# Kernel tuning notes

Measured on AMD Instinct MI355X. Metric: run time of the kernel, lower is better.

Reference implementation:

```python
import jax, jax.numpy as jnp
import numpy as np
from jax import lax

N, C, H, W = 1, 3, 480, 640
K_LCN = 9
K_ASW = 12
SIGMA_OMEGA = 2.0
LCN_WEIGHT = 0.5
OCC_WEIGHT = 0.1
LN2 = 0.6931


def _box_filter(x, k):
    # depthwise kxk mean filter, zero ('same') padding — matches F.conv2d(groups=3)
    w = jnp.ones((C, 1, k, k), x.dtype) / (k * k)
    return lax.conv_general_dilated(
        x, w, (1, 1), [(k // 2, k // 2)] * 2,
        dimension_numbers=('NCHW', 'OIHW', 'NCHW'), feature_group_count=C)


def _lcn(img, k=K_LCN):
    mean = _box_filter(img, k)
    msq = _box_filter(img ** 2, k)
    std = jnp.sqrt(jax.nn.relu(msq - mean ** 2)) * (k * k) / (k * k - 1)
    return (img - mean) / (std + 1e-5), std


def _sample_x(img, x):
    # grid_sample with identity y and x-only shift reduces to horizontal linear
    # interpolation with zero padding (align_corners=False pixel-center math).
    Wd = img.shape[-1]
    x0 = jnp.floor(x)
    w1 = x - x0
    x0i = x0.astype(jnp.int32)
    def gather(xi):
        valid = ((xi >= 0) & (xi < Wd)).astype(img.dtype)
        return jnp.take_along_axis(img, jnp.clip(xi, 0, Wd - 1), axis=-1) * valid
    return gather(x0i) * (1 - w1) + gather(x0i + 1) * w1


def _resample(img, disp_other, disp_guide, sign):
    # sample img and disp_other at x = j + sign*disp_guide (left view: sign=-1)
    xs = jnp.arange(W, dtype=img.dtype) + sign * disp_guide  # [N,1,H,W]
    recon_img = _sample_x(img, jnp.broadcast_to(xs, img.shape))
    recon_disp = _sample_x(disp_other, xs)
    return recon_img, recon_disp


def _asw(guide, cost, k=K_ASW, sigma=SIGMA_OMEGA):
    # adaptive support-weight (bilateral) aggregation over a kxk window,
    # zero-padded, window offsets -k//2 .. k//2-1 (even k, as in the original)
    pad = k // 2
    gp = jnp.pad(guide, ((0, 0), (0, 0), (pad, pad), (pad, pad)))
    cp = jnp.pad(cost, ((0, 0), (0, 0), (pad, pad), (pad, pad)))
    shape = guide.shape
    def body(carry, idx):
        wg, ca = carry
        i = idx // k
        j = idx % k
        gs = lax.dynamic_slice(gp, (0, 0, i, j), shape)
        cs = lax.dynamic_slice(cp, (0, 0, i, j), shape)
        t = jnp.exp(-jnp.abs(guide - gs) / sigma)
        return (wg + t, ca + t * cs), None
    init = (jnp.zeros(shape, guide.dtype), jnp.zeros(shape, guide.dtype))
    (wg, ca), _ = lax.scan(body, init, jnp.arange(k * k, dtype=jnp.int32))
    return ca / wg


def _ce_ones_target(p):
    # CrossEntropyLoss(mean) with logits [1-p, p] and target class 1 everywhere
    logits = jnp.concatenate([1.0 - p, p], axis=1)  # [N,2,H,W]
    ls = jax.nn.log_softmax(logits, axis=1)
    return -jnp.mean(ls[:, 1])


def _forward(left_img, right_img, dispmap_left, dispmap_right, weight):
    recon_img_right, recon_disp_right = _resample(right_img, dispmap_right, dispmap_left, -1.0)
    recon_img_left, recon_disp_left = _resample(left_img, dispmap_left, dispmap_right, 1.0)

    losses_left_photo = jnp.abs(left_img - recon_img_right)
    losses_right_photo = jnp.abs(right_img - recon_img_left)

    rir_lcn, _ = _lcn(recon_img_right)
    ril_lcn, _ = _lcn(recon_img_left)
    l_lcn, l_std = _lcn(left_img)
    r_lcn, r_std = _lcn(right_img)
    losses_left_lcn = _asw(left_img, jnp.abs((l_lcn - rir_lcn) * l_std))
    # NOTE: original uses left_img as the ASW guide for the right loss too
    losses_right_lcn = _asw(left_img, jnp.abs((r_lcn - ril_lcn) * r_std))

    losses_left = (1 - LCN_WEIGHT) * losses_left_photo + LCN_WEIGHT * losses_left_lcn
    losses_right = (1 - LCN_WEIGHT) * losses_right_photo + LCN_WEIGHT * losses_right_lcn

    p_left = jnp.exp(-LN2 * jnp.abs(dispmap_left - recon_disp_right))   # [N,1,H,W]
    p_right = jnp.exp(-LN2 * jnp.abs(dispmap_right - recon_disp_left))

    loss_invalid = _ce_ones_target(p_left) + _ce_ones_target(p_right)

    mask_left = (p_left > 0.5).astype(losses_left.dtype)    # broadcasts over C=3
    mask_right = (p_right > 0.5).astype(losses_right.dtype)
    loss_valid = (jnp.sum(losses_left * mask_left) / (C * jnp.sum(mask_left) + 1e-6)
                  + jnp.sum(losses_right * mask_right) / (C * jnp.sum(mask_right) + 1e-6))

    return weight * ((1 - OCC_WEIGHT) * loss_valid + OCC_WEIGHT * loss_invalid)


def setup_inputs() -> dict:
    key = jax.random.key(0)
    k1, k2, k3, k4, k5 = jax.random.split(key, 5)
    return {
        'left_img': jax.random.uniform(k1, (N, C, H, W), dtype=jnp.float32),
        'right_img': jax.random.uniform(k2, (N, C, H, W), dtype=jnp.float32),
        'dispmap_left': jax.random.uniform(k3, (N, 1, H, W), dtype=jnp.float32) * 32.0,
        'dispmap_right': jax.random.uniform(k4, (N, 1, H, W), dtype=jnp.float32) * 32.0,
        'dispmap_gt': jax.random.uniform(k5, (N, 1, H, W), dtype=jnp.float32) * 32.0,
        'brk': 0,
        'weight': jnp.asarray(1.0, dtype=jnp.float32),
    }


def reference(left_img, right_img, dispmap_left, dispmap_right, dispmap_gt, brk, weight):
    # dispmap_gt and brk are accepted but unused by the original forward math
    return _forward(left_img, right_img, dispmap_left, dispmap_right, weight)
```

## Files before the change

### kernel.cpp

```cpp
#include <hip/hip_runtime.h>
#include <math.h>

#define HH 480
#define WW 640
#define HW (HH*WW)

#define NB1 1200
#define NB3 3600

__device__ __forceinline__ unsigned bf16rne(float f) {
    unsigned u = __float_as_uint(f);
    return (u + 0x7fffu + ((u >> 16) & 1u)) >> 16;
}


__device__ __forceinline__ float sample1(const float* __restrict__ row, float x) {
    float x0 = floorf(x);
    float w1 = x - x0;
    int xi = (int)x0;
    float v0 = (xi >= 0 && xi < WW) ? row[xi] : 0.f;
    float v1 = (xi + 1 >= 0 && xi + 1 < WW) ? row[xi + 1] : 0.f;
    return v0 * (1.f - w1) + v1 * w1;
}

__global__ __launch_bounds__(256) void k_resample(
    const float* __restrict__ left, const float* __restrict__ right,
    const float* __restrict__ dispL, const float* __restrict__ dispR,
    float* __restrict__ rir, float* __restrict__ ril,
    unsigned char* __restrict__ maskb, float* __restrict__ part1)
{
    __shared__ float red[4][6];
    int tid = threadIdx.x;
    int idx = blockIdx.x * blockDim.x + tid;
    int h = idx / WW;
    int w = idx - h * WW;
    float dL = dispL[idx];
    float dR = dispR[idx];
    float xl = (float)w - dL;
    float xr = (float)w + dR;
    float photoL = 0.f, photoR = 0.f;
    #pragma unroll
    for (int c = 0; c < 3; ++c) {
        float rv = sample1(right + c*HW + h*WW, xl);
        float lv = sample1(left  + c*HW + h*WW, xr);
        rir[c*HW + idx] = rv;
        ril[c*HW + idx] = lv;
        photoL += fabsf(left [c*HW + idx] - rv);
        photoR += fabsf(right[c*HW + idx] - lv);
    }
    float rdr = sample1(dispR + h*WW, xl);
    float rdl = sample1(dispL + h*WW, xr);
    float pl = __expf(-0.6931f * fabsf(dL - rdr));
    float pr = __expf(-0.6931f * fabsf(dR - rdl));
    float mL = (pl > 0.5f) ? 1.f : 0.f;
    float mR = (pr > 0.5f) ? 1.f : 0.f;
    maskb[idx] = (unsigned char)((mL > 0.f ? 1u : 0u) | (mR > 0.f ? 2u : 0u));

    float vals[6];
    vals[0] = 0.5f * photoL * mL;
    vals[1] = mL;
    vals[2] = 0.5f * photoR * mR;
    vals[3] = mR;
    vals[4] = log1pf(__expf(1.f - 2.f * pl));
    vals[5] = log1pf(__expf(1.f - 2.f * pr));

    int lane = tid & 63, wave = tid >> 6;
    #pragma unroll
    for (int k = 0; k < 6; ++k) {
        float v = vals[k];
        #pragma unroll
        for (int off = 32; off > 0; off >>= 1) v += __shfl_down(v, off);
        if (lane == 0) red[wave][k] = v;
    }
    __syncthreads();
    if (tid < 6)
        part1[blockIdx.x * 8 + tid] =
            red[0][tid] + red[1][tid] + red[2][tid] + red[3][tid];
}


__global__ __launch_bounds__(256) void k_lcnpack(
    const float* __restrict__ left, const float* __restrict__ right,
    const float* __restrict__ rir, const float* __restrict__ ril,
    unsigned* __restrict__ epem,
    unsigned short* __restrict__ cl16, unsigned short* __restrict__ cr16)
{
    __shared__ float raw[2][16][40];
    __shared__ float2 hsp[2][16][32];
    int tx = threadIdx.x, ty = threadIdx.y;
    int tid = ty * 32 + tx;
    int gx0 = blockIdx.x * 32, gy0 = blockIdx.y * 8;
    int side = blockIdx.z & 1, ch = blockIdx.z >> 1;
    const float* __restrict__ A = (side ? right : left) + ch*HW;
    const float* __restrict__ B = (side ? ril   : rir) + ch*HW;

    for (int e = tid; e < 2*16*40; e += 256) {
        int a   = e / 640;
        int rem = e - a * 640;
        int r   = rem / 40;
        int x   = rem - r * 40;
        int gy = gy0 + r - 4, gx = gx0 + x - 4;
        float v = 0.f;
        if ((unsigned)gy < (unsigned)HH && (unsigned)gx < (unsigned)WW)
            v = (a ? B : A)[gy*WW + gx];
        ((float*)raw)[e] = v;
    }
    __syncthreads();

    {
        int f   = tid;
        int a   = f >> 7;
        int rem = f & 127;
        int r   = rem >> 3;
        int x0  = (rem & 7) * 4;
        const float* row = &raw[a][r][x0];
        float4 p0 = *(const float4*)(row);
        float4 p1 = *(const float4*)(row + 4);
        float4 p2 = *(const float4*)(row + 8);
        float v[12] = {p0.x, p0.y, p0.z, p0.w, p1.x, p1.y, p1.z, p1.w,
                       p2.x, p2.y, p2.z, p2.w};
        float sq[12];
        #pragma unroll
        for (int i = 0; i < 12; ++i) sq[i] = v[i] * v[i];
        float s0 = v[0]+v[1]+v[2]+v[3]+v[4]+v[5]+v[6]+v[7]+v[8];
        float q0 = sq[0]+sq[1]+sq[2]+sq[3]+sq[4]+sq[5]+sq[6]+sq[7]+sq[8];
        float s1 = s0 - v[0] + v[9];
        float q1 = q0 - sq[0] + sq[9];
        float s2 = s1 - v[1] + v[10];
        float q2 = q1 - sq[1] + sq[10];
        float s3 = s2 - v[2] + v[11];
        float q3 = q2 - sq[2] + sq[11];
        float4* out = (float4*)&hsp[a][r][x0];
        out[0] = make_float4(s0, q0, s1, q1);
        out[1] = make_float4(s2, q2, s3, q3);
    }
    __syncthreads();

    int idx = ch*HW + (gy0 + ty) * WW + gx0 + tx;
    float SA = 0.f, SA2 = 0.f, SB = 0.f, SB2 = 0.f;
    #pragma unroll
    for (int dy = 0; dy < 9; ++dy) {
        float2 ha = hsp[0][ty + dy][tx];
        float2 hb = hsp[1][ty + dy][tx];
        SA  += ha.x;
        SA2 += ha.y;
        SB  += hb.x;
        SB2 += hb.y;
    }
    float meanA = SA * (1.f/81.f);
    float stdA  = sqrtf(fmaxf(SA2 * (1.f/81.f) - meanA * meanA, 0.f)) * (81.f/80.f);
    float lcnA  = (raw[0][ty + 4][tx + 4] - meanA) / (stdA + 1e-5f);
    float meanB = SB * (1.f/81.f);
    float stdB  = sqrtf(fmaxf(SB2 * (1.f/81.f) - meanB * meanB, 0.f)) * (81.f/80.f);
    float lcnB  = (raw[1][ty + 4][tx + 4] - meanB) / (stdB + 1e-5f);
    float cost  = fabsf((lcnA - lcnB) * stdA);
    if (side == 0) {
        float g = raw[0][ty + 4][tx + 4];
        epem[idx] = bf16rne(__expf(0.5f * g)) | (bf16rne(__expf(-0.5f * g)) << 16);
        cl16[idx] = (unsigned short)bf16rne(cost);
    } else {
        cr16[idx] = (unsigned short)bf16rne(cost);
    }
}


#define T3H 19
#define T3W 43

__global__ __launch_bounds__(64) void k_asw_reduce(
    const unsigned* __restrict__ epem,
    const unsigned short* __restrict__ cl16, const unsigned short* __restrict__ cr16,
    const unsigned char* __restrict__ maskb,
    float* __restrict__ part3)
{
    __shared__ float4 tile[T3H][T3W];
    int tx = threadIdx.x, ty = threadIdx.y;
    int tid = tx + 32 * ty;
    int c = blockIdx.z;
    int gx0 = blockIdx.x * 32, gy0 = blockIdx.y * 8;

    for (int e = tid; e < T3H * T3W; e += 64) {
        int r   = e / T3W;
        int x   = e - r * T3W;
        int gy = gy0 + r - 6, gx = gx0 + x - 6;
        float4 v = make_float4(1.f, 1.f, 0.f, 0.f);
        if ((unsigned)gy < (unsigned)HH && (unsigned)gx < (unsigned)WW) {
            int o = c*HW + gy*WW + gx;
            unsigned pe = epem[o];
            v.x = __uint_as_float(pe << 16);
            v.y = __uint_as_float(pe & 0xffff0000u);
            v.z = __uint_as_float((unsigned)cl16[o] << 16);
            v.w = __uint_as_float((unsigned)cr16[o] << 16);
        }
        tile[r][x] = v;
    }
    __syncthreads();

    int ty4 = 4 * ty;
    float epc[4], emc[4];
    #pragma unroll
    for (int i = 0; i < 4; ++i) {
        float4 cv = tile[ty4 + i + 6][tx + 6];
        epc[i] = cv.x;
        emc[i] = cv.y;
    }

    float wg[4] = {0.f,0.f,0.f,0.f}, aL[4] = {0.f,0.f,0.f,0.f}, aR[4] = {0.f,0.f,0.f,0.f};

    auto taprow = [&](int kap, int i0, int i1) {
        const float4* row = &tile[ty4 + kap][tx];
        #pragma unroll
        for (int dx = 0; dx < 12; ++dx) {
            float4 v = row[dx];
            #pragma unroll
            for (int i = 0; i < 4; ++i) {
                if (i >= i0 && i <= i1) {
                    float t = fminf(emc[i] * v.x, epc[i] * v.y);
                    wg[i] += t;
                    aL[i] = fmaf(t, v.z, aL[i]);
                    aR[i] = fmaf(t, v.w, aR[i]);
                }
            }
        }
    };

    taprow(0, 0, 0);
    taprow(1, 0, 1);
    taprow(2, 0, 2);
    for (int kap = 3; kap <= 11; ++kap)
        taprow(kap, 0, 3);
    taprow(12, 1, 3);
    taprow(13, 2, 3);
    taprow(14, 3, 3);

    float v0 = 0.f, v2 = 0.f;
    #pragma unroll
    for (int i = 0; i < 4; ++i) {
        int idx = (gy0 + ty4 + i) * WW + gx0 + tx;
        unsigned m = maskb[idx];
        float aswL = aL[i] / wg[i];
        float aswR = aR[i] / wg[i];
        if (m & 1u) v0 += 0.5f * aswL;
        if (m & 2u) v2 += 0.5f * aswR;
    }

    #pragma unroll
    for (int off = 32; off > 0; off >>= 1) {
        v0 += __shfl_down(v0, off);
        v2 += __shfl_down(v2, off);
    }
    if (tid == 0) {
        int bid = (blockIdx.z * gridDim.y + blockIdx.y) * gridDim.x + blockIdx.x;
        part3[bid * 8 + 0] = v0;
        part3[bid * 8 + 1] = v2;
    }
}


__global__ __launch_bounds__(256) void k_final(
    const float* __restrict__ part1, const float* __restrict__ part3,
    const float* __restrict__ weight, float* __restrict__ out)
{
    __shared__ float red[4][6];
    int tid = threadIdx.x;
    float v[6] = {0.f, 0.f, 0.f, 0.f, 0.f, 0.f};
    for (int b = tid; b < NB1; b += 256) {
        #pragma unroll
        for (int k = 0; k < 6; ++k) v[k] += part1[b * 8 + k];
    }
    for (int b = tid; b < NB3; b += 256) {
        v[0] += part3[b * 8 + 0];
        v[2] += part3[b * 8 + 1];
    }
    int lane = tid & 63, wave = tid >> 6;
    #pragma unroll
    for (int k = 0; k < 6; ++k) {
        float s = v[k];
        #pragma unroll
        for (int off = 32; off > 0; off >>= 1) s += __shfl_down(s, off);
        if (lane == 0) red[wave][k] = s;
    }
    __syncthreads();
    if (tid == 0) {
        float a[6];
        #pragma unroll
        for (int k = 0; k < 6; ++k)
            a[k] = red[0][k] + red[1][k] + red[2][k] + red[3][k];
        float loss_valid = a[0] / (3.f * a[1] + 1e-6f) + a[2] / (3.f * a[3] + 1e-6f);
        float loss_invalid = (a[4] + a[5]) * (1.f / (float)HW);
        out[0] = weight[0] * (0.9f * loss_valid + 0.1f * loss_invalid);
    }
}


extern "C" void kernel_launch(void* const* d_in, const int* in_sizes, int n_in,
                              void* d_out, int out_size, void* d_ws, size_t ws_size,
                              hipStream_t stream)
{
    const float* left  = (const float*)d_in[0];
    const float* right = (const float*)d_in[1];
    const float* dispL = (const float*)d_in[2];
    const float* dispR = (const float*)d_in[3];
    const float* weight = (const float*)d_in[6];

    float* ws    = (float*)d_ws;
    float* rir   = ws;
    float* ril   = rir + 3*HW;
    unsigned* epem = (unsigned*)(ws + 6*HW);
    unsigned short* cl16 = (unsigned short*)(ws + 9*HW);
    unsigned short* cr16 = (unsigned short*)(ws + 9*HW) + 3*HW;
    unsigned char* maskb = (unsigned char*)(ws + 12*HW);
    float* part1 = ws + 12*HW + HW/4;
    float* part3 = part1 + NB1*8;

    k_resample<<<NB1, 256, 0, stream>>>(left, right, dispL, dispR, rir, ril, maskb, part1);

    dim3 blk2(32, 8);
    dim3 grd2(WW / 32, HH / 8, 6);
    k_lcnpack<<<grd2, blk2, 0, stream>>>(left, right, rir, ril, epem, cl16, cr16);

    dim3 blk3(32, 2);
    dim3 grd3(WW / 32, HH / 8, 3);
    k_asw_reduce<<<grd3, blk3, 0, stream>>>(epem, cl16, cr16, maskb, part3);

    k_final<<<1, 256, 0, stream>>>(part1, part3, weight, (float*)d_out);
}
```

Measured before the change: 75.83 us.

## Compute two adjacent columns per thread with packed float2 math in ASW reduce

Each ASW thread now handles two horizontally adjacent output pixels, using two-wide vector types so the window arithmetic can map to packed FP32 instructions. Each loaded tile element is reused by both columns. The shared tile is split by even and odd columns so the two-column access pattern stays conflict-friendly. The block covers 32x16 pixels, which halves the number of blocks and enlarges the halo rows, at the cost of more registers per thread.

```diff
diff --git a/kernel.cpp b/kernel.cpp
--- a/kernel.cpp
+++ b/kernel.cpp
@@ -6,7 +6,9 @@
 #define HW (HH*WW)
 
 #define NB1 1200
-#define NB3 3600
+#define NB3 1800
+
+typedef float v2f __attribute__((ext_vector_type(2)));
 
 __device__ __forceinline__ unsigned bf16rne(float f) {
     unsigned u = __float_as_uint(f);
@@ -164,8 +166,7 @@
 }
 
 
-#define T3H 19
-#define T3W 43
+#define T3H 27
 
 __global__ __launch_bounds__(64) void k_asw_reduce(
     const unsigned* __restrict__ epem,
@@ -173,15 +174,15 @@
     const unsigned char* __restrict__ maskb,
     float* __restrict__ part3)
 {
-    __shared__ float4 tile[T3H][T3W];
+    __shared__ float4 tile[2][T3H][22];
     int tx = threadIdx.x, ty = threadIdx.y;
-    int tid = tx + 32 * ty;
+    int tid = tx + 16 * ty;
     int c = blockIdx.z;
-    int gx0 = blockIdx.x * 32, gy0 = blockIdx.y * 8;
-
-    for (int e = tid; e < T3H * T3W; e += 64) {
-        int r   = e / T3W;
-        int x   = e - r * T3W;
+    int gx0 = blockIdx.x * 32, gy0 = blockIdx.y * 16;
+
+    for (int e = tid; e < T3H * 43; e += 64) {
+        int r = e / 43;
+        int x = e - r * 43;
         int gy = gy0 + r - 6, gx = gx0 + x - 6;
         float4 v = make_float4(1.f, 1.f, 0.f, 0.f);
         if ((unsigned)gy < (unsigned)HH && (unsigned)gx < (unsigned)WW) {
@@ -192,33 +193,62 @@
             v.z = __uint_as_float((unsigned)cl16[o] << 16);
             v.w = __uint_as_float((unsigned)cr16[o] << 16);
         }
-        tile[r][x] = v;
+        tile[x & 1][r][x >> 1] = v;
     }
     __syncthreads();
 
     int ty4 = 4 * ty;
-    float epc[4], emc[4];
+    v2f epc[4], emc[4];
     #pragma unroll
     for (int i = 0; i < 4; ++i) {
-        float4 cv = tile[ty4 + i + 6][tx + 6];
-        epc[i] = cv.x;
-        emc[i] = cv.y;
-    }
-
-    float wg[4] = {0.f,0.f,0.f,0.f}, aL[4] = {0.f,0.f,0.f,0.f}, aR[4] = {0.f,0.f,0.f,0.f};
+        float4 c0 = tile[0][ty4 + i + 6][3 + tx];
+        float4 c1 = tile[1][ty4 + i + 6][3 + tx];
+        epc[i] = (v2f){c0.x, c1.x};
+        emc[i] = (v2f){c0.y, c1.y};
+    }
+
+    v2f wg[4] = {{0.f,0.f},{0.f,0.f},{0.f,0.f},{0.f,0.f}};
+    v2f aL[4] = {{0.f,0.f},{0.f,0.f},{0.f,0.f},{0.f,0.f}};
+    v2f aR[4] = {{0.f,0.f},{0.f,0.f},{0.f,0.f},{0.f,0.f}};
 
     auto taprow = [&](int kap, int i0, int i1) {
-        const float4* row = &tile[ty4 + kap][tx];
-        #pragma unroll
-        for (int dx = 0; dx < 12; ++dx) {
-            float4 v = row[dx];
+        int r = ty4 + kap;
+        {
+            float4 v = tile[0][r][tx];
             #pragma unroll
             for (int i = 0; i < 4; ++i) {
                 if (i >= i0 && i <= i1) {
-                    float t = fminf(emc[i] * v.x, epc[i] * v.y);
+                    float t = fminf(emc[i].x * v.x, epc[i].x * v.y);
+                    wg[i].x += t;
+                    aL[i].x = fmaf(t, v.z, aL[i].x);
+                    aR[i].x = fmaf(t, v.w, aR[i].x);
+                }
+            }
+        }
+        #pragma unroll
+        for (int dx = 1; dx <= 11; ++dx) {
+            float4 v = tile[dx & 1][r][tx + (dx >> 1)];
+            v2f ep = {v.x, v.x}, em = {v.y, v.y};
+            v2f cl = {v.z, v.z}, cr = {v.w, v.w};
+            #pragma unroll
+            for (int i = 0; i < 4; ++i) {
+                if (i >= i0 && i <= i1) {
+                    v2f t = __builtin_elementwise_min(emc[i] * ep, epc[i] * em);
                     wg[i] += t;
-                    aL[i] = fmaf(t, v.z, aL[i]);
-                    aR[i] = fmaf(t, v.w, aR[i]);
+                    aL[i] = __builtin_elementwise_fma(t, cl, aL[i]);
+                    aR[i] = __builtin_elementwise_fma(t, cr, aR[i]);
+                }
+            }
+        }
+        {
+            float4 v = tile[0][r][tx + 6];
+            #pragma unroll
+            for (int i = 0; i < 4; ++i) {
+                if (i >= i0 && i <= i1) {
+                    float t = fminf(emc[i].y * v.x, epc[i].y * v.y);
+                    wg[i].y += t;
+                    aL[i].y = fmaf(t, v.z, aL[i].y);
+                    aR[i].y = fmaf(t, v.w, aR[i].y);
                 }
             }
         }
@@ -236,12 +266,16 @@
     float v0 = 0.f, v2 = 0.f;
     #pragma unroll
     for (int i = 0; i < 4; ++i) {
-        int idx = (gy0 + ty4 + i) * WW + gx0 + tx;
-        unsigned m = maskb[idx];
-        float aswL = aL[i] / wg[i];
-        float aswR = aR[i] / wg[i];
-        if (m & 1u) v0 += 0.5f * aswL;
-        if (m & 2u) v2 += 0.5f * aswR;
+        #pragma unroll
+        for (int h = 0; h < 2; ++h) {
+            int idx = (gy0 + ty4 + i) * WW + gx0 + 2 * tx + h;
+            unsigned m = maskb[idx];
+            float w_ = h ? wg[i].y : wg[i].x;
+            float l_ = h ? aL[i].y : aL[i].x;
+            float r_ = h ? aR[i].y : aR[i].x;
+            if (m & 1u) v0 += 0.5f * (l_ / w_);
+            if (m & 2u) v2 += 0.5f * (r_ / w_);
+        }
     }
 
     #pragma unroll
@@ -319,8 +353,8 @@
     dim3 grd2(WW / 32, HH / 8, 6);
     k_lcnpack<<<grd2, blk2, 0, stream>>>(left, right, rir, ril, epem, cl16, cr16);
 
-    dim3 blk3(32, 2);
-    dim3 grd3(WW / 32, HH / 8, 3);
+    dim3 blk3(16, 4);
+    dim3 grd3(WW / 32, HH / 16, 3);
     k_asw_reduce<<<grd3, blk3, 0, stream>>>(epem, cl16, cr16, maskb, part3);
 
     k_final<<<1, 256, 0, stream>>>(part1, part3, weight, (float*)d_out);
```

New measurement: 78.79 us. +3.9%, slower.
